# Performance work log

Measured on AMD Instinct MI355X. Metric: run time of the kernel, lower is better.

The kernel has to match this reference:

```python
import jax, jax.numpy as jnp
import numpy as np

B, T, E, H, C = 32, 128, 256, 256, 16

def setup_inputs() -> dict:
    key = jax.random.key(0)
    ks = jax.random.split(key, 16)
    def p(k, shape, scale=0.05):
        return jax.random.normal(k, shape, dtype=jnp.float32) * scale
    return {
        "x": jax.random.normal(ks[0], (B, T, E), dtype=jnp.float32),
        "W_in": p(ks[1], (H, E)), "b_in": p(ks[2], (H,)),
        "Wih": p(ks[3], (3 * H, H)), "bih": p(ks[4], (3 * H,)),
        "Whh": p(ks[5], (3 * H, H)), "bhh": p(ks[6], (3 * H,)),
        "Wa": p(ks[7], (H, H)), "ba": p(ks[8], (H,)),
        "Ua": p(ks[9], (H, H)), "ub": p(ks[10], (H,)),
        "va_w": p(ks[11], (1, H)), "va_b": p(ks[12], (1,)),
        "Wo": p(ks[13], (C, 2 * H)), "bo": p(ks[14], (C,)),
    }

def reference(x, W_in, b_in, Wih, bih, Whh, bhh, Wa, ba, Ua, ub, va_w, va_b, Wo, bo):
    # linear_in (+ Identity activation): x -> [B,T,H]
    xp = x @ W_in.T + b_in
    xp_t = jnp.transpose(xp, (1, 0, 2))          # [T,B,H], time-major
    # Precompute per-step GRU input projections and attention key projections
    xw = xp_t @ Wih.T + bih                      # [T,B,3H]
    uax = xp_t @ Ua.T + ub                       # [T,B,H]
    ts = jnp.arange(T)

    def gru_step(h, xw_t):
        # PyTorch GRU cell: gate order r, z, n
        hw = h @ Whh.T + bhh                     # [B,3H]
        xr, xz, xn = jnp.split(xw_t, 3, axis=-1)
        hr, hz, hn = jnp.split(hw, 3, axis=-1)
        r = jax.nn.sigmoid(xr + hr)
        z = jax.nn.sigmoid(xz + hz)
        n = jnp.tanh(xn + r * hn)
        return (1.0 - z) * n + z * h

    def outer_step(h_prev, i):
        # Re-run RNN over prefix x[:, :i+1] starting from the CARRIED hidden,
        # exactly as the torch loop does (hidden is not reset between iters).
        def inner(h, inp):
            t, xw_t = inp
            hn = gru_step(h, xw_t)
            h = jnp.where(t <= i, hn, h)         # freeze past the prefix end
            return h, h
        h_last, outs = jax.lax.scan(inner, h_prev, (ts, xw))  # outs [T,B,H]
        # Bahdanau attention: query = rnn outputs, keys = linear_in outputs
        s = jnp.tanh(outs @ Wa.T + ba + uax)     # [T,B,H]
        scores = jnp.squeeze(s @ va_w.T, -1) + va_b  # [T,B]
        scores = jnp.where((ts <= i)[:, None], scores, -1e9)
        w = jax.nn.softmax(scores, axis=0)       # softmax over prefix positions
        context = jnp.einsum('tb,tbh->bh', w, xp_t)
        cats = jnp.concatenate([h_last, context], axis=-1)  # [B,2H]
        return h_last, cats @ Wo.T + bo          # logits [B,C]

    h0 = jnp.zeros((x.shape[0], H), dtype=x.dtype)
    _, logits = jax.lax.scan(outer_step, h0, ts)  # [T,B,C]
    return jax.nn.sigmoid(jnp.transpose(logits, (1, 0, 2)))  # [B,T,C]
```

## Files before the change

kernel.cpp:

```cpp
#include <hip/hip_runtime.h>

constexpr int NB = 32;
constexpr int NT = 128;
constexpr int NE = 256;
constexpr int NH = 256;
constexpr int NC = 16;

typedef _Float16 f16;
typedef f16 f16x2 __attribute__((ext_vector_type(2)));
typedef f16 f16x8 __attribute__((ext_vector_type(8)));

__device__ __forceinline__ float sigmoidf_(float x) {
    return 1.f / (1.f + __expf(-x));
}
__device__ __forceinline__ float tanhf_(float x) {
    x = fminf(fmaxf(x, -15.f), 15.f);
    float e = __expf(-2.f * x);
    return (1.f - e) / (1.f + e);
}
__device__ __forceinline__ float dot4_(float4 a, float4 b) {
    return a.x * b.x + a.y * b.y + a.z * b.z + a.w * b.w;
}
#if __has_builtin(__builtin_amdgcn_fdot2)
__device__ __forceinline__ float fdot2_(f16x2 a, f16x2 b, float c) {
    return __builtin_amdgcn_fdot2(a, b, c, false);
}
#else
__device__ __forceinline__ float fdot2_(f16x2 a, f16x2 b, float c) {
    return (float)a[0] * (float)b[0] + (float)a[1] * (float)b[1] + c;
}
#endif
#define PAIR(v, k) __builtin_shufflevector((v), (v), (k), (k) + 1)

__global__ __launch_bounds__(256) void k_lin_in(
    const float* __restrict__ x, const float* __restrict__ W_in,
    const float* __restrict__ b_in, float* __restrict__ xp) {
    const int tb = blockIdx.x;
    const int t = tb >> 5, b = tb & 31;
    const int tid = threadIdx.x;
    __shared__ __align__(16) float xl[NE];
    xl[tid] = x[(b * NT + t) * NE + tid];
    __syncthreads();
    const float* __restrict__ wr = W_in + tid * NE;
    float acc = b_in[tid];
#pragma unroll 8
    for (int k = 0; k < NE; k += 4)
        acc += dot4_(*(const float4*)(wr + k), *(const float4*)(xl + k));
    xp[tb * NH + tid] = acc;
}

__global__ __launch_bounds__(256) void k_proj(
    const float* __restrict__ xp, const float* __restrict__ Wih,
    const float* __restrict__ bih, const float* __restrict__ Ua,
    const float* __restrict__ ub, float* __restrict__ xw,
    float* __restrict__ uax) {
    const int tb = blockIdx.x;
    const int tid = threadIdx.x;
    __shared__ __align__(16) float xl[NH];
    xl[tid] = xp[tb * NH + tid];
    __syncthreads();
    const float* __restrict__ wr = Wih + tid * NH;
    const float* __restrict__ wz = Wih + (NH + tid) * NH;
    const float* __restrict__ wn = Wih + (2 * NH + tid) * NH;
    const float* __restrict__ wu = Ua + tid * NH;
    float ar = bih[tid], az = bih[NH + tid], an = bih[2 * NH + tid], au = ub[tid];
#pragma unroll 4
    for (int k = 0; k < NH; k += 4) {
        float4 xv = *(const float4*)(xl + k);
        ar += dot4_(*(const float4*)(wr + k), xv);
        az += dot4_(*(const float4*)(wz + k), xv);
        an += dot4_(*(const float4*)(wn + k), xv);
        au += dot4_(*(const float4*)(wu + k), xv);
    }
    float* xwp = xw + tb * (3 * NH);
    xwp[tid] = ar;
    xwp[NH + tid] = az;
    xwp[2 * NH + tid] = an;
    uax[tb * NH + tid] = au;
}

__global__ __launch_bounds__(256) void k_pack(
    const float* __restrict__ Whh, const float* __restrict__ Wa,
    f16x8* __restrict__ Wpk, f16x8* __restrict__ Wak) {
    const int id = blockIdx.x * 256 + threadIdx.x;
    if (id < 32 * 768) {
        const int kc = id / 768, row = id % 768;
        const float* src = Whh + row * NH + kc * 8;
        f16x8 v;
#pragma unroll
        for (int m = 0; m < 8; ++m) v[m] = (f16)src[m];
        Wpk[id] = v;
    } else {
        const int id2 = id - 32 * 768;
        const int kc = id2 >> 8, row = id2 & 255;
        const float* src = Wa + row * NH + kc * 8;
        f16x8 v;
#pragma unroll
        for (int m = 0; m < 8; ++m) v[m] = (f16)src[m];
        Wak[id2] = v;
    }
}

__global__ __attribute__((amdgpu_flat_work_group_size(1024, 1024),
                          amdgpu_waves_per_eu(4)))
void k_chain(
    const float* __restrict__ Whh, const float* __restrict__ bhh,
    const float* __restrict__ xw, float* __restrict__ Hc) {
    const int b = blockIdx.x;
    const int tid = threadIdx.x;
    const int j = tid >> 2, c = tid & 3;
    const int wv = tid >> 6, lane = tid & 63;

    __shared__ __align__(16) f16x8 WnL[8 * 16 * 64];
    __shared__ __align__(16) f16 hb[2][4 * 72];

    for (int idx = tid; idx < 8192; idx += 1024) {
        const int s = idx >> 10, w = (idx >> 6) & 15, ln = idx & 63;
        const int row = w * 16 + (ln >> 2), c2 = ln & 3;
        const float* src = Whh + (size_t)(2 * NH + row) * NH + c2 * 64 + s * 8;
        f16x8 v;
#pragma unroll
        for (int m = 0; m < 8; ++m) v[m] = (f16)src[m];
        WnL[idx] = v;
    }
    f16x2 wr[32], wz[32];
    {
        const float2* pr = (const float2*)(Whh + (size_t)(0 * NH + j) * NH + c * 64);
        const float2* pz = (const float2*)(Whh + (size_t)(1 * NH + j) * NH + c * 64);
#pragma unroll
        for (int m = 0; m < 32; ++m) {
            float2 a = pr[m]; wr[m] = f16x2{(f16)a.x, (f16)a.y};
            float2 d = pz[m]; wz[m] = f16x2{(f16)d.x, (f16)d.y};
        }
    }
    const float bhr = bhh[j], bhz = bhh[NH + j], bhn = bhh[2 * NH + j];
    if (tid < NH) hb[0][(tid >> 6) * 72 + (tid & 63)] = (f16)0.f;
    float hprev = 0.f;
    int cur = 0;

    const f16x8* __restrict__ wn8 = WnL + wv * 64 + lane;
    const float* __restrict__ xwB = xw + (size_t)b * 3 * NH;

    float xr = xwB[j], xz = xwB[NH + j], xn = xwB[2 * NH + j];
    __syncthreads();

#pragma unroll 1
    for (int i = 0; i < NT; ++i) {
#pragma unroll 1
        for (int t = 0; t <= i; ++t) {
            const int tn = (t < i) ? t + 1 : 0;
            const float* __restrict__ xwn = xw + (size_t)(tn * NB + b) * (3 * NH);
            const float nxr = xwn[j], nxz = xwn[NH + j], nxn = xwn[2 * NH + j];

            const f16* hc = hb[cur] + c * 72;
            float ar = 0.f, az = 0.f, an = 0.f;
#pragma unroll
            for (int s = 0; s < 8; ++s) {
                const f16x8 hv = *(const f16x8*)(hc + s * 8);
                const f16x8 wn_ = wn8[s * 1024];
                const f16x2 h0 = PAIR(hv, 0), h1 = PAIR(hv, 2),
                            h2 = PAIR(hv, 4), h3 = PAIR(hv, 6);
                ar = fdot2_(wr[s * 4 + 0], h0, ar);
                ar = fdot2_(wr[s * 4 + 1], h1, ar);
                ar = fdot2_(wr[s * 4 + 2], h2, ar);
                ar = fdot2_(wr[s * 4 + 3], h3, ar);
                az = fdot2_(wz[s * 4 + 0], h0, az);
                az = fdot2_(wz[s * 4 + 1], h1, az);
                az = fdot2_(wz[s * 4 + 2], h2, az);
                az = fdot2_(wz[s * 4 + 3], h3, az);
                an = fdot2_(PAIR(wn_, 0), h0, an);
                an = fdot2_(PAIR(wn_, 2), h1, an);
                an = fdot2_(PAIR(wn_, 4), h2, an);
                an = fdot2_(PAIR(wn_, 6), h3, an);
            }
            ar += __shfl_xor(ar, 1); ar += __shfl_xor(ar, 2);
            az += __shfl_xor(az, 1); az += __shfl_xor(az, 2);
            an += __shfl_xor(an, 1); an += __shfl_xor(an, 2);
            const float r = sigmoidf_(xr + ar + bhr);
            const float z = sigmoidf_(xz + az + bhz);
            const float n = tanhf_(xn + r * (an + bhn));
            const float hnew = (1.f - z) * n + z * hprev;
            hprev = hnew;
            if (c == 0) {
                hb[cur ^ 1][(j >> 6) * 72 + (j & 63)] = (f16)hnew;
                if (t == i) Hc[((size_t)i * NB + b) * NH + j] = hnew;
            }
            xr = nxr; xz = nxz; xn = nxn;
            cur ^= 1;
            __syncthreads();
        }
    }
}

__global__ __launch_bounds__(512) void k_attn(
    const float* __restrict__ Hc, const float* __restrict__ xw,
    const float* __restrict__ uax, const float* __restrict__ xp,
    const f16x8* __restrict__ Wpk, const f16x8* __restrict__ Wak,
    const float* __restrict__ bhh, const float* __restrict__ ba,
    const float* __restrict__ va_w, const float* __restrict__ Wo,
    const float* __restrict__ bo, float* __restrict__ out) {
    const int b  = blockIdx.x >> 3;
    const int bk = blockIdx.x & 7;
    const int tid = threadIdx.x;
    const int col = tid >> 1, c = tid & 1;
    const int lane = tid & 63, wid = tid >> 6;

    __shared__ __align__(16) float S[16][NH];
    __shared__ __align__(16) f16 Sh[16][NH];
    __shared__ float red1[8][16];
    __shared__ float mL[16], lL[16], aL[16], eL[16];
    __shared__ float redH[8][256];

    const float bhr = bhh[col], bhz = bhh[NH + col], bhn = bhh[2 * NH + col];
    const float ba_j = ba[col], va_j = va_w[col];
    float ctx[16];
#pragma unroll
    for (int u = 0; u < 16; ++u) {
        const int ic = bk + 8 * u;
        const float hv = (ic == 0) ? 0.f : Hc[((size_t)(ic - 1) * NB + b) * NH + col];
        if (c == 0) { S[u][col] = hv; Sh[u][col] = (f16)hv; }
        ctx[u] = 0.f;
    }
    if (tid < 16) { mL[tid] = -1e30f; lL[tid] = 0.f; }
    __syncthreads();

    const int imax = bk + 8 * 15;
#pragma unroll 1
    for (int t = 0; t <= imax; ++t) {
        const size_t base = (size_t)(t * NB + b);
        const float xr = xw[base * 3 * NH + col];
        const float xz = xw[base * 3 * NH + NH + col];
        const float xn = xw[base * 3 * NH + 2 * NH + col];
        const float ux = uax[base * NH + col];
        const float xpt = xp[base * NH + col];

        float ar[16], az[16], an[16];
#pragma unroll
        for (int u = 0; u < 16; ++u) { ar[u] = 0.f; az[u] = 0.f; an[u] = 0.f; }
        {
            int kc = c;
            f16x8 wR = Wpk[kc * 768 + col];
            f16x8 wZ = Wpk[kc * 768 + 256 + col];
            f16x8 wN = Wpk[kc * 768 + 512 + col];
#pragma unroll 1
            for (int kk = 0; kk < 16; ++kk) {
                const int kcn = kc + 2;
                f16x8 nR, nZ, nN;
                if (kk < 15) {
                    nR = Wpk[kcn * 768 + col];
                    nZ = Wpk[kcn * 768 + 256 + col];
                    nN = Wpk[kcn * 768 + 512 + col];
                }
#pragma unroll
                for (int u = 0; u < 16; ++u) {
                    if (bk + 8 * u < t) continue;
                    const f16x8 hv = *(const f16x8*)&Sh[u][kc * 8];
                    const f16x2 h0 = PAIR(hv, 0), h1 = PAIR(hv, 2),
                                h2 = PAIR(hv, 4), h3 = PAIR(hv, 6);
                    ar[u] = fdot2_(PAIR(wR, 0), h0, ar[u]);
                    ar[u] = fdot2_(PAIR(wR, 2), h1, ar[u]);
                    ar[u] = fdot2_(PAIR(wR, 4), h2, ar[u]);
                    ar[u] = fdot2_(PAIR(wR, 6), h3, ar[u]);
                    az[u] = fdot2_(PAIR(wZ, 0), h0, az[u]);
                    az[u] = fdot2_(PAIR(wZ, 2), h1, az[u]);
                    az[u] = fdot2_(PAIR(wZ, 4), h2, az[u]);
                    az[u] = fdot2_(PAIR(wZ, 6), h3, az[u]);
                    an[u] = fdot2_(PAIR(wN, 0), h0, an[u]);
                    an[u] = fdot2_(PAIR(wN, 2), h1, an[u]);
                    an[u] = fdot2_(PAIR(wN, 4), h2, an[u]);
                    an[u] = fdot2_(PAIR(wN, 6), h3, an[u]);
                }
                wR = nR; wZ = nZ; wN = nN; kc = kcn;
            }
        }
        float hn[16];
#pragma unroll
        for (int u = 0; u < 16; ++u) {
            if (bk + 8 * u < t) continue;
            float arf = ar[u] + __shfl_xor(ar[u], 1);
            float azf = az[u] + __shfl_xor(az[u], 1);
            float anf = an[u] + __shfl_xor(an[u], 1);
            const float r = sigmoidf_(xr + arf + bhr);
            const float z = sigmoidf_(xz + azf + bhz);
            const float n = tanhf_(xn + r * (anf + bhn));
            hn[u] = (1.f - z) * n + z * S[u][col];
        }
        __syncthreads();
#pragma unroll
        for (int u = 0; u < 16; ++u) {
            if (bk + 8 * u < t) continue;
            if (c == 0) { S[u][col] = hn[u]; Sh[u][col] = (f16)hn[u]; }
        }
        __syncthreads();

        float sc[16];
#pragma unroll
        for (int u = 0; u < 16; ++u) sc[u] = 0.f;
        {
            int kc = c;
            f16x8 wA = Wak[kc * 256 + col];
#pragma unroll 1
            for (int kk = 0; kk < 16; ++kk) {
                const int kcn = kc + 2;
                f16x8 nA;
                if (kk < 15) nA = Wak[kcn * 256 + col];
#pragma unroll
                for (int u = 0; u < 16; ++u) {
                    if (bk + 8 * u < t) continue;
                    const f16x8 hv = *(const f16x8*)&Sh[u][kc * 8];
                    sc[u] = fdot2_(PAIR(wA, 0), PAIR(hv, 0), sc[u]);
                    sc[u] = fdot2_(PAIR(wA, 2), PAIR(hv, 2), sc[u]);
                    sc[u] = fdot2_(PAIR(wA, 4), PAIR(hv, 4), sc[u]);
                    sc[u] = fdot2_(PAIR(wA, 6), PAIR(hv, 6), sc[u]);
                }
                wA = nA; kc = kcn;
            }
        }
#pragma unroll
        for (int u = 0; u < 16; ++u) {
            if (bk + 8 * u < t) continue;
            const float sv = sc[u] + __shfl_xor(sc[u], 1);
            float p = (c == 0) ? va_j * tanhf_(sv + ba_j + ux) : 0.f;
#pragma unroll
            for (int off = 32; off; off >>= 1) p += __shfl_xor(p, off);
            if (lane == 0) red1[wid][u] = p;
        }
        __syncthreads();
        if (tid < 16 && bk + 8 * tid >= t) {
            float s = 0.f;
#pragma unroll
            for (int w = 0; w < 8; ++w) s += red1[w][tid];
            const float mo = mL[tid];
            const float mn = fmaxf(mo, s);
            const float e  = __expf(s - mn);
            const float al = __expf(mo - mn);
            lL[tid] = lL[tid] * al + e;
            mL[tid] = mn; aL[tid] = al; eL[tid] = e;
        }
        __syncthreads();
#pragma unroll
        for (int u = 0; u < 16; ++u) {
            if (bk + 8 * u < t) continue;
            ctx[u] = ctx[u] * aL[u] + eL[u] * xpt;
        }
    }

#pragma unroll 1
    for (int u = 0; u < 16; ++u) {
        const float hl = S[u][col];
        const float cx = ctx[u] / lL[u];
#pragma unroll
        for (int cls = 0; cls < NC; ++cls) {
            float p = Wo[cls * (2 * NH) + col] * hl + Wo[cls * (2 * NH) + NH + col] * cx;
            p = (c == 0) ? p : 0.f;
#pragma unroll
            for (int off = 32; off; off >>= 1) p += __shfl_xor(p, off);
            if (lane == 0) redH[wid][u * 16 + cls] = p;
        }
    }
    __syncthreads();
    if (tid < 256) {
        const int u = tid >> 4, cls = tid & 15;
        const int ic = bk + 8 * u;
        float lg = bo[cls];
#pragma unroll
        for (int w = 0; w < 8; ++w) lg += redH[w][tid];
        out[((size_t)b * NT + ic) * NC + cls] = sigmoidf_(lg);
    }
}

extern "C" void kernel_launch(void* const* d_in, const int* in_sizes, int n_in,
                              void* d_out, int out_size, void* d_ws, size_t ws_size,
                              hipStream_t stream) {
    (void)in_sizes; (void)n_in; (void)out_size; (void)ws_size;
    const float* x    = (const float*)d_in[0];
    const float* W_in = (const float*)d_in[1];
    const float* b_in = (const float*)d_in[2];
    const float* Wih  = (const float*)d_in[3];
    const float* bih  = (const float*)d_in[4];
    const float* Whh  = (const float*)d_in[5];
    const float* bhh  = (const float*)d_in[6];
    const float* Wa   = (const float*)d_in[7];
    const float* ba   = (const float*)d_in[8];
    const float* Ua   = (const float*)d_in[9];
    const float* ub   = (const float*)d_in[10];
    const float* va_w = (const float*)d_in[11];
    const float* Wo   = (const float*)d_in[13];
    const float* bo   = (const float*)d_in[14];
    float* out = (float*)d_out;

    float* ws  = (float*)d_ws;
    float* xp  = ws;
    float* xw  = xp  + (size_t)NT * NB * NH;
    float* uax = xw  + (size_t)NT * NB * 3 * NH;
    float* Hc  = uax + (size_t)NT * NB * NH;
    f16x8* Wpk = (f16x8*)(Hc + (size_t)NT * NB * NH);
    f16x8* Wak = Wpk + 32 * 768;

    hipLaunchKernelGGL(k_lin_in, dim3(NT * NB), dim3(256), 0, stream, x, W_in, b_in, xp);
    hipLaunchKernelGGL(k_proj,   dim3(NT * NB), dim3(256), 0, stream, xp, Wih, bih, Ua, ub, xw, uax);
    hipLaunchKernelGGL(k_pack,   dim3(128),     dim3(256), 0, stream, Whh, Wa, Wpk, Wak);
    hipLaunchKernelGGL(k_chain,  dim3(NB),      dim3(1024), 0, stream, Whh, bhh, xw, Hc);
    hipLaunchKernelGGL(k_attn,   dim3(NB * 8),  dim3(512), 0, stream,
                       Hc, xw, uax, xp, Wpk, Wak, bhh, ba, va_w, Wo, bo, out);
}
```

Baseline: 17.00 ms.

## Halve recurrent chain block size and store part of Whh as FP8 in LDS

The sequential GRU chain kernel now runs 512 threads per batch (2 per hidden unit instead of 4), each with a 128-wide slice of the hidden state. The z-gate weights stay fully in registers as f16, while the n-gate weights and half of the r-gate weights are pre-encoded to scaled FP8 (E4M3-style, ×64) by a new packing kernel and stored in LDS. They are decoded to f16 on the fly, using a hardware conversion builtin if available. The aim is to cut block-wide barrier and shuffle-reduction cost per serial step and fit all weights on chip with fewer threads. The cost is reduced weight precision and extra decode work per step.

Result: slower. 26.06 ms (+53.3%).

```diff
diff --git a/kernel.cpp b/kernel.cpp
--- a/kernel.cpp
+++ b/kernel.cpp
@@ -31,6 +31,38 @@
 }
 #endif
 #define PAIR(v, k) __builtin_shufflevector((v), (v), (k), (k) + 1)
+
+#if __has_builtin(__builtin_amdgcn_cvt_pk_f16_fp8)
+#define FP8_HW 1
+__device__ __forceinline__ void dec4_(unsigned int d, f16x2& a, f16x2& b) {
+    a = __builtin_bit_cast(f16x2, __builtin_amdgcn_cvt_pk_f16_fp8((short)(d & 0xffffu)));
+    b = __builtin_bit_cast(f16x2, __builtin_amdgcn_cvt_pk_f16_fp8((short)(d >> 16)));
+}
+#else
+#define FP8_HW 0
+__device__ __forceinline__ void dec4_(unsigned int d, f16x2& a, f16x2& b) {
+    unsigned int ev = d & 0x00ff00ffu;
+    unsigned int od = (d >> 8) & 0x00ff00ffu;
+    unsigned int ea = (((ev & 0x007f007fu) << 7) + 0x20002000u) | ((ev & 0x00800080u) << 8);
+    unsigned int eb = (((od & 0x007f007fu) << 7) + 0x20002000u) | ((od & 0x00800080u) << 8);
+    a = __builtin_bit_cast(f16x2, ea);
+    b = __builtin_bit_cast(f16x2, eb);
+}
+#endif
+
+__device__ __forceinline__ unsigned char enc8_(float w) {
+    const float f = w * 64.f;
+    const unsigned int b = __builtin_bit_cast(unsigned int, f);
+    const unsigned int sgn = (b >> 24) & 0x80u;
+    unsigned int mag = b & 0x7fffffffu;
+    if (mag < 0x3c800000u) return (unsigned char)(sgn | 0x08u);
+    if (mag > 0x43e00000u) mag = 0x43e00000u;
+    unsigned int base = mag >> 20;
+    const unsigned int rem = mag & 0xfffffu;
+    base += (rem > 0x80000u) || (rem == 0x80000u && (base & 1u));
+    if (base > 1086u) base = 1086u;
+    return (unsigned char)(sgn | (base - 960u));
+}
 
 __global__ __launch_bounds__(256) void k_lin_in(
     const float* __restrict__ x, const float* __restrict__ W_in,
@@ -101,48 +133,73 @@
     }
 }
 
-__global__ __attribute__((amdgpu_flat_work_group_size(1024, 1024),
-                          amdgpu_waves_per_eu(4)))
-void k_chain(
+__global__ __launch_bounds__(256) void k_pack8(
+    const float* __restrict__ Whh, unsigned char* __restrict__ wsn,
+    unsigned char* __restrict__ wsr) {
+    const int id = blockIdx.x * 256 + threadIdx.x;
+    const bool isN = id < 8192;
+    const int g = isN ? id : id - 8192;
+    const int s = g >> 9, wvl = g & 511;
+    const int j = wvl >> 1, c = wvl & 1;
+    const int row = isN ? (2 * NH + j) : j;
+    const int kbase = isN ? (c * 128 + s * 8) : (c * 128 + 64 + s * 8);
+    const float* src = Whh + (size_t)row * NH + kbase;
+    unsigned char out[8];
+#pragma unroll
+    for (int dw = 0; dw < 2; ++dw)
+#pragma unroll
+        for (int p = 0; p < 4; ++p) {
+#if FP8_HW
+            const int koff = p;
+#else
+            const int koff = (p == 1) ? 2 : (p == 2) ? 1 : p;
+#endif
+            out[dw * 4 + p] = enc8_(src[dw * 4 + koff]);
+        }
+        unsigned char* dst = (isN ? wsn : wsr) + (size_t)g * 8;
+#pragma unroll
+    for (int m = 0; m < 8; ++m) dst[m] = out[m];
+}
+
+__global__ __launch_bounds__(512) void k_chain(
     const float* __restrict__ Whh, const float* __restrict__ bhh,
-    const float* __restrict__ xw, float* __restrict__ Hc) {
+    const float* __restrict__ xw, const unsigned char* __restrict__ wsn,
+    const unsigned char* __restrict__ wsr, float* __restrict__ Hc) {
     const int b = blockIdx.x;
     const int tid = threadIdx.x;
-    const int j = tid >> 2, c = tid & 3;
+    const int j = tid >> 1, c = tid & 1;
     const int wv = tid >> 6, lane = tid & 63;
 
-    __shared__ __align__(16) f16x8 WnL[8 * 16 * 64];
-    __shared__ __align__(16) f16 hb[2][4 * 72];
-
-    for (int idx = tid; idx < 8192; idx += 1024) {
-        const int s = idx >> 10, w = (idx >> 6) & 15, ln = idx & 63;
-        const int row = w * 16 + (ln >> 2), c2 = ln & 3;
-        const float* src = Whh + (size_t)(2 * NH + row) * NH + c2 * 64 + s * 8;
-        f16x8 v;
-#pragma unroll
-        for (int m = 0; m < 8; ++m) v[m] = (f16)src[m];
-        WnL[idx] = v;
-    }
-    f16x2 wr[32], wz[32];
+    __shared__ __align__(16) uint2 WnL[16 * 8 * 64];
+    __shared__ __align__(16) uint2 WrL[8 * 8 * 64];
+    __shared__ __align__(16) f16 hb[2][NH];
+
     {
-        const float2* pr = (const float2*)(Whh + (size_t)(0 * NH + j) * NH + c * 64);
-        const float2* pz = (const float2*)(Whh + (size_t)(1 * NH + j) * NH + c * 64);
-#pragma unroll
-        for (int m = 0; m < 32; ++m) {
-            float2 a = pr[m]; wr[m] = f16x2{(f16)a.x, (f16)a.y};
-            float2 d = pz[m]; wz[m] = f16x2{(f16)d.x, (f16)d.y};
-        }
+        const uint2* srcn = (const uint2*)wsn;
+        const uint2* srcr = (const uint2*)wsr;
+        for (int idx = tid; idx < 8192; idx += 512) WnL[idx] = srcn[idx];
+        for (int idx = tid; idx < 4096; idx += 512) WrL[idx] = srcr[idx];
+    }
+    f16x2 wz[64], wrA[32];
+    {
+        const float2* pz = (const float2*)(Whh + (size_t)(NH + j) * NH + c * 128);
+        const float2* pr = (const float2*)(Whh + (size_t)j * NH + c * 128);
+#pragma unroll
+        for (int m = 0; m < 64; ++m) { float2 v = pz[m]; wz[m] = f16x2{(f16)v.x, (f16)v.y}; }
+#pragma unroll
+        for (int m = 0; m < 32; ++m) { float2 v = pr[m]; wrA[m] = f16x2{(f16)v.x, (f16)v.y}; }
     }
     const float bhr = bhh[j], bhz = bhh[NH + j], bhn = bhh[2 * NH + j];
-    if (tid < NH) hb[0][(tid >> 6) * 72 + (tid & 63)] = (f16)0.f;
+    if (tid < NH) hb[0][tid] = (f16)0.f;
     float hprev = 0.f;
     int cur = 0;
-
-    const f16x8* __restrict__ wn8 = WnL + wv * 64 + lane;
     const float* __restrict__ xwB = xw + (size_t)b * 3 * NH;
-
     float xr = xwB[j], xz = xwB[NH + j], xn = xwB[2 * NH + j];
     __syncthreads();
+
+    const uint2* __restrict__ wn8 = WnL + wv * 64 + lane;
+    const uint2* __restrict__ wr8 = WrL + wv * 64 + lane;
+    constexpr float S8 = 1.f / 64.f;
 
 #pragma unroll 1
     for (int i = 0; i < NT; ++i) {
@@ -152,37 +209,67 @@
             const float* __restrict__ xwn = xw + (size_t)(tn * NB + b) * (3 * NH);
             const float nxr = xwn[j], nxz = xwn[NH + j], nxn = xwn[2 * NH + j];
 
-            const f16* hc = hb[cur] + c * 72;
-            float ar = 0.f, az = 0.f, an = 0.f;
+            const f16* hc = hb[cur] + c * 128;
+            float arA = 0.f, arB = 0.f, az = 0.f, an = 0.f;
 #pragma unroll
             for (int s = 0; s < 8; ++s) {
                 const f16x8 hv = *(const f16x8*)(hc + s * 8);
-                const f16x8 wn_ = wn8[s * 1024];
+                const uint2 nw = wn8[s * 512];
+                f16x2 n0, n1, n2, n3;
+                dec4_(nw.x, n0, n1);
+                dec4_(nw.y, n2, n3);
                 const f16x2 h0 = PAIR(hv, 0), h1 = PAIR(hv, 2),
                             h2 = PAIR(hv, 4), h3 = PAIR(hv, 6);
-                ar = fdot2_(wr[s * 4 + 0], h0, ar);
-                ar = fdot2_(wr[s * 4 + 1], h1, ar);
-                ar = fdot2_(wr[s * 4 + 2], h2, ar);
-                ar = fdot2_(wr[s * 4 + 3], h3, ar);
+                arA = fdot2_(wrA[s * 4 + 0], h0, arA);
+                arA = fdot2_(wrA[s * 4 + 1], h1, arA);
+                arA = fdot2_(wrA[s * 4 + 2], h2, arA);
+                arA = fdot2_(wrA[s * 4 + 3], h3, arA);
                 az = fdot2_(wz[s * 4 + 0], h0, az);
                 az = fdot2_(wz[s * 4 + 1], h1, az);
                 az = fdot2_(wz[s * 4 + 2], h2, az);
                 az = fdot2_(wz[s * 4 + 3], h3, az);
-                an = fdot2_(PAIR(wn_, 0), h0, an);
-                an = fdot2_(PAIR(wn_, 2), h1, an);
-                an = fdot2_(PAIR(wn_, 4), h2, an);
-                an = fdot2_(PAIR(wn_, 6), h3, an);
+                an = fdot2_(n0, h0, an);
+                an = fdot2_(n1, h1, an);
+                an = fdot2_(n2, h2, an);
+                an = fdot2_(n3, h3, an);
             }
-            ar += __shfl_xor(ar, 1); ar += __shfl_xor(ar, 2);
-            az += __shfl_xor(az, 1); az += __shfl_xor(az, 2);
-            an += __shfl_xor(an, 1); an += __shfl_xor(an, 2);
+#pragma unroll
+            for (int s = 8; s < 16; ++s) {
+                const f16x8 hv = *(const f16x8*)(hc + s * 8);
+                const uint2 nw = wn8[s * 512];
+                const uint2 rw = wr8[(s - 8) * 512];
+                f16x2 n0, n1, n2, n3, r0, r1, r2, r3;
+                dec4_(nw.x, n0, n1);
+                dec4_(nw.y, n2, n3);
+                dec4_(rw.x, r0, r1);
+                dec4_(rw.y, r2, r3);
+                const f16x2 h0 = PAIR(hv, 0), h1 = PAIR(hv, 2),
+                            h2 = PAIR(hv, 4), h3 = PAIR(hv, 6);
+                arB = fdot2_(r0, h0, arB);
+                arB = fdot2_(r1, h1, arB);
+                arB = fdot2_(r2, h2, arB);
+                arB = fdot2_(r3, h3, arB);
+                az = fdot2_(wz[s * 4 + 0], h0, az);
+                az = fdot2_(wz[s * 4 + 1], h1, az);
+                az = fdot2_(wz[s * 4 + 2], h2, az);
+                az = fdot2_(wz[s * 4 + 3], h3, az);
+                an = fdot2_(n0, h0, an);
+                an = fdot2_(n1, h1, an);
+                an = fdot2_(n2, h2, an);
+                an = fdot2_(n3, h3, an);
+            }
+            const float myar = arA + arB * S8;
+            const float ar = myar + __shfl_xor(myar, 1);
+            const float azf = az + __shfl_xor(az, 1);
+            const float anp = an + __shfl_xor(an, 1);
+            const float anf = anp * S8;
             const float r = sigmoidf_(xr + ar + bhr);
-            const float z = sigmoidf_(xz + az + bhz);
-            const float n = tanhf_(xn + r * (an + bhn));
+            const float z = sigmoidf_(xz + azf + bhz);
+            const float n = tanhf_(xn + r * (anf + bhn));
             const float hnew = (1.f - z) * n + z * hprev;
             hprev = hnew;
             if (c == 0) {
-                hb[cur ^ 1][(j >> 6) * 72 + (j & 63)] = (f16)hnew;
+                hb[cur ^ 1][j] = (f16)hnew;
                 if (t == i) Hc[((size_t)i * NB + b) * NH + j] = hnew;
             }
             xr = nxr; xz = nxz; xn = nxn;
@@ -396,11 +483,14 @@
     float* Hc  = uax + (size_t)NT * NB * NH;
     f16x8* Wpk = (f16x8*)(Hc + (size_t)NT * NB * NH);
     f16x8* Wak = Wpk + 32 * 768;
+    unsigned char* wsn = (unsigned char*)(Wak + 32 * 256);
+    unsigned char* wsr = wsn + 16 * 8 * 64 * 8;
 
     hipLaunchKernelGGL(k_lin_in, dim3(NT * NB), dim3(256), 0, stream, x, W_in, b_in, xp);
     hipLaunchKernelGGL(k_proj,   dim3(NT * NB), dim3(256), 0, stream, xp, Wih, bih, Ua, ub, xw, uax);
     hipLaunchKernelGGL(k_pack,   dim3(128),     dim3(256), 0, stream, Whh, Wa, Wpk, Wak);
-    hipLaunchKernelGGL(k_chain,  dim3(NB),      dim3(1024), 0, stream, Whh, bhh, xw, Hc);
+    hipLaunchKernelGGL(k_pack8,  dim3(48),      dim3(256), 0, stream, Whh, wsn, wsr);
+    hipLaunchKernelGGL(k_chain,  dim3(NB),      dim3(512), 0, stream, Whh, bhh, xw, wsn, wsr, Hc);
     hipLaunchKernelGGL(k_attn,   dim3(NB * 8),  dim3(512), 0, stream,
                        Hc, xw, uax, xp, Wpk, Wak, bhh, ba, va_w, Wo, bo, out);
 }
```

## Quantize GRU r and n recurrent weights to 8-bit floats held in LDS

Applied to the files above, without the earlier changes.

Adds a pack kernel that rounds the r and n gate rows of Whh to an 8-bit format: fp16 with the low mantissa byte dropped (1 sign, 5 exponent, 2 mantissa bits). The recurrent chain kernel keeps these compact weights in shared memory and expands them to fp16 pairs with byte permutes before the dot products. Only the z gate stays in registers as fp16. This frees the registers that held the r weights and halves the LDS traffic for the n weights, with the aim of cheapening the serial per-step inner loop. The cost is a large loss of weight precision, which may push the outputs outside the accuracy tolerance, plus extra permute instructions per step.

After: 20.03 ms. 17.9% more time.

```diff
diff --git a/kernel.cpp b/kernel.cpp
--- a/kernel.cpp
+++ b/kernel.cpp
@@ -31,6 +31,25 @@
 }
 #endif
 #define PAIR(v, k) __builtin_shufflevector((v), (v), (k), (k) + 1)
+
+#if __has_builtin(__builtin_amdgcn_perm)
+__device__ __forceinline__ void decq_(unsigned int d, f16x2& a, f16x2& b) {
+    a = __builtin_bit_cast(f16x2, __builtin_amdgcn_perm(d, 0u, 0x05000400u));
+    b = __builtin_bit_cast(f16x2, __builtin_amdgcn_perm(d, 0u, 0x07000600u));
+}
+#else
+__device__ __forceinline__ void decq_(unsigned int d, f16x2& a, f16x2& b) {
+    a = __builtin_bit_cast(f16x2, ((d << 8) & 0x0000FF00u) | ((d << 16) & 0xFF000000u));
+    b = __builtin_bit_cast(f16x2, ((d >> 8) & 0x0000FF00u) | (d & 0xFF000000u));
+}
+#endif
+
+__device__ __forceinline__ unsigned char enc5_(float w) {
+    const unsigned short h = __builtin_bit_cast(unsigned short, (f16)w);
+    unsigned int u = (unsigned int)h;
+    u = u + 0x7Fu + ((u >> 8) & 1u);
+    return (unsigned char)(u >> 8);
+}
 
 __global__ __launch_bounds__(256) void k_lin_in(
     const float* __restrict__ x, const float* __restrict__ W_in,
@@ -101,46 +120,58 @@
     }
 }
 
-__global__ __attribute__((amdgpu_flat_work_group_size(1024, 1024),
-                          amdgpu_waves_per_eu(4)))
-void k_chain(
+__global__ __launch_bounds__(256) void k_pack8(
+    const float* __restrict__ Whh, uint4* __restrict__ wsr8,
+    uint4* __restrict__ wsn8) {
+    const int id = blockIdx.x * 256 + threadIdx.x;
+    const int gate = id >> 12;
+    const int g = id & 4095;
+    const int s2 = g >> 10, tv = g & 1023;
+    const int j = tv >> 2, cc = tv & 3;
+    const int row = (gate == 0) ? j : (2 * NH + j);
+    const float* src = Whh + (size_t)row * NH + cc * 64 + s2 * 16;
+    unsigned int w[4];
+#pragma unroll
+    for (int q = 0; q < 4; ++q) {
+        unsigned int v = 0;
+#pragma unroll
+        for (int m = 0; m < 4; ++m)
+            v |= (unsigned int)enc5_(src[q * 4 + m]) << (8 * m);
+        w[q] = v;
+    }
+    (gate == 0 ? wsr8 : wsn8)[g] = uint4{w[0], w[1], w[2], w[3]};
+}
+
+__global__ __launch_bounds__(1024) void k_chain(
     const float* __restrict__ Whh, const float* __restrict__ bhh,
-    const float* __restrict__ xw, float* __restrict__ Hc) {
+    const float* __restrict__ xw, const uint4* __restrict__ wsr8,
+    const uint4* __restrict__ wsn8, float* __restrict__ Hc) {
     const int b = blockIdx.x;
     const int tid = threadIdx.x;
     const int j = tid >> 2, c = tid & 3;
-    const int wv = tid >> 6, lane = tid & 63;
-
-    __shared__ __align__(16) f16x8 WnL[8 * 16 * 64];
+
+    __shared__ __align__(16) uint4 Wr4[4 * 1024];
+    __shared__ __align__(16) uint4 Wn4[4 * 1024];
     __shared__ __align__(16) f16 hb[2][4 * 72];
 
-    for (int idx = tid; idx < 8192; idx += 1024) {
-        const int s = idx >> 10, w = (idx >> 6) & 15, ln = idx & 63;
-        const int row = w * 16 + (ln >> 2), c2 = ln & 3;
-        const float* src = Whh + (size_t)(2 * NH + row) * NH + c2 * 64 + s * 8;
-        f16x8 v;
-#pragma unroll
-        for (int m = 0; m < 8; ++m) v[m] = (f16)src[m];
-        WnL[idx] = v;
-    }
-    f16x2 wr[32], wz[32];
+    for (int idx = tid; idx < 4096; idx += 1024) {
+        Wr4[idx] = wsr8[idx];
+        Wn4[idx] = wsn8[idx];
+    }
+    f16x2 wz[32];
     {
-        const float2* pr = (const float2*)(Whh + (size_t)(0 * NH + j) * NH + c * 64);
-        const float2* pz = (const float2*)(Whh + (size_t)(1 * NH + j) * NH + c * 64);
+        const float2* pz = (const float2*)(Whh + (size_t)(NH + j) * NH + c * 64);
 #pragma unroll
         for (int m = 0; m < 32; ++m) {
-            float2 a = pr[m]; wr[m] = f16x2{(f16)a.x, (f16)a.y};
-            float2 d = pz[m]; wz[m] = f16x2{(f16)d.x, (f16)d.y};
+            float2 v = pz[m];
+            wz[m] = f16x2{(f16)v.x, (f16)v.y};
         }
     }
     const float bhr = bhh[j], bhz = bhh[NH + j], bhn = bhh[2 * NH + j];
     if (tid < NH) hb[0][(tid >> 6) * 72 + (tid & 63)] = (f16)0.f;
     float hprev = 0.f;
     int cur = 0;
-
-    const f16x8* __restrict__ wn8 = WnL + wv * 64 + lane;
     const float* __restrict__ xwB = xw + (size_t)b * 3 * NH;
-
     float xr = xwB[j], xz = xwB[NH + j], xn = xwB[2 * NH + j];
     __syncthreads();
 
@@ -155,23 +186,32 @@
             const f16* hc = hb[cur] + c * 72;
             float ar = 0.f, az = 0.f, an = 0.f;
 #pragma unroll
-            for (int s = 0; s < 8; ++s) {
-                const f16x8 hv = *(const f16x8*)(hc + s * 8);
-                const f16x8 wn_ = wn8[s * 1024];
-                const f16x2 h0 = PAIR(hv, 0), h1 = PAIR(hv, 2),
-                            h2 = PAIR(hv, 4), h3 = PAIR(hv, 6);
-                ar = fdot2_(wr[s * 4 + 0], h0, ar);
-                ar = fdot2_(wr[s * 4 + 1], h1, ar);
-                ar = fdot2_(wr[s * 4 + 2], h2, ar);
-                ar = fdot2_(wr[s * 4 + 3], h3, ar);
-                az = fdot2_(wz[s * 4 + 0], h0, az);
-                az = fdot2_(wz[s * 4 + 1], h1, az);
-                az = fdot2_(wz[s * 4 + 2], h2, az);
-                az = fdot2_(wz[s * 4 + 3], h3, az);
-                an = fdot2_(PAIR(wn_, 0), h0, an);
-                an = fdot2_(PAIR(wn_, 2), h1, an);
-                an = fdot2_(PAIR(wn_, 4), h2, an);
-                an = fdot2_(PAIR(wn_, 6), h3, an);
+            for (int s2 = 0; s2 < 4; ++s2) {
+                const uint4 rq = Wr4[s2 * 1024 + tid];
+                const uint4 nq = Wn4[s2 * 1024 + tid];
+                const f16x8 hv0 = *(const f16x8*)(hc + s2 * 16);
+                const f16x8 hv1 = *(const f16x8*)(hc + s2 * 16 + 8);
+                const f16x2 p0 = PAIR(hv0, 0), p1 = PAIR(hv0, 2),
+                            p2 = PAIR(hv0, 4), p3 = PAIR(hv0, 6);
+                const f16x2 p4 = PAIR(hv1, 0), p5 = PAIR(hv1, 2),
+                            p6 = PAIR(hv1, 4), p7 = PAIR(hv1, 6);
+                az = fdot2_(wz[s2 * 8 + 0], p0, az);
+                az = fdot2_(wz[s2 * 8 + 1], p1, az);
+                az = fdot2_(wz[s2 * 8 + 2], p2, az);
+                az = fdot2_(wz[s2 * 8 + 3], p3, az);
+                az = fdot2_(wz[s2 * 8 + 4], p4, az);
+                az = fdot2_(wz[s2 * 8 + 5], p5, az);
+                az = fdot2_(wz[s2 * 8 + 6], p6, az);
+                az = fdot2_(wz[s2 * 8 + 7], p7, az);
+                f16x2 da, db;
+                decq_(rq.x, da, db); ar = fdot2_(da, p0, ar); ar = fdot2_(db, p1, ar);
+                decq_(rq.y, da, db); ar = fdot2_(da, p2, ar); ar = fdot2_(db, p3, ar);
+                decq_(rq.z, da, db); ar = fdot2_(da, p4, ar); ar = fdot2_(db, p5, ar);
+                decq_(rq.w, da, db); ar = fdot2_(da, p6, ar); ar = fdot2_(db, p7, ar);
+                decq_(nq.x, da, db); an = fdot2_(da, p0, an); an = fdot2_(db, p1, an);
+                decq_(nq.y, da, db); an = fdot2_(da, p2, an); an = fdot2_(db, p3, an);
+                decq_(nq.z, da, db); an = fdot2_(da, p4, an); an = fdot2_(db, p5, an);
+                decq_(nq.w, da, db); an = fdot2_(da, p6, an); an = fdot2_(db, p7, an);
             }
             ar += __shfl_xor(ar, 1); ar += __shfl_xor(ar, 2);
             az += __shfl_xor(az, 1); az += __shfl_xor(az, 2);
@@ -396,11 +436,14 @@
     float* Hc  = uax + (size_t)NT * NB * NH;
     f16x8* Wpk = (f16x8*)(Hc + (size_t)NT * NB * NH);
     f16x8* Wak = Wpk + 32 * 768;
+    uint4* wsr8 = (uint4*)(Wak + 32 * 256);
+    uint4* wsn8 = wsr8 + 4096;
 
     hipLaunchKernelGGL(k_lin_in, dim3(NT * NB), dim3(256), 0, stream, x, W_in, b_in, xp);
     hipLaunchKernelGGL(k_proj,   dim3(NT * NB), dim3(256), 0, stream, xp, Wih, bih, Ua, ub, xw, uax);
     hipLaunchKernelGGL(k_pack,   dim3(128),     dim3(256), 0, stream, Whh, Wa, Wpk, Wak);
-    hipLaunchKernelGGL(k_chain,  dim3(NB),      dim3(1024), 0, stream, Whh, bhh, xw, Hc);
+    hipLaunchKernelGGL(k_pack8,  dim3(32),      dim3(256), 0, stream, Whh, wsr8, wsn8);
+    hipLaunchKernelGGL(k_chain,  dim3(NB),      dim3(1024), 0, stream, Whh, bhh, xw, wsr8, wsn8, Hc);
     hipLaunchKernelGGL(k_attn,   dim3(NB * 8),  dim3(512), 0, stream,
                        Hc, xw, uax, xp, Wpk, Wak, bhh, ba, va_w, Wo, bo, out);
 }
```
